# Kernel tuning notes

Hardware: AMD Instinct MI355X
Metric: run time of the kernel (lower is better)

## Reference

```python
import jax, jax.numpy as jnp
import numpy as np

NUM_GROUPS = 32
EPS = 1e-6


def group_norm(x, gamma, beta):
    # x: [b, c, n]
    b, c, n = x.shape
    xg = x.reshape(b, NUM_GROUPS, (c // NUM_GROUPS) * n)
    mean = xg.mean(axis=-1, keepdims=True)
    var = xg.var(axis=-1, keepdims=True)
    xg = (xg - mean) * jax.lax.rsqrt(var + EPS)
    x = xg.reshape(b, c, n)
    return x * gamma[None, :, None] + beta[None, :, None]


def conv1x1(x, w, bias):
    # x: [b, c, n], w: [out, in], bias: [out]
    return jnp.einsum('oc,bcn->bon', w, x) + bias[None, :, None]


def setup_inputs() -> dict:
    key = jax.random.key(0)
    ks = jax.random.split(key, 12)
    b, c, n = 16, 512, 2048
    scale = 1.0 / np.sqrt(c)
    inp = {
        'x': jax.random.normal(ks[0], (b, c, n), dtype=jnp.float32),
        'gn_gamma': jnp.ones((c,), dtype=jnp.float32),
        'gn_beta': jnp.zeros((c,), dtype=jnp.float32),
        'wq': jax.random.normal(ks[1], (c, c), dtype=jnp.float32) * scale,
        'bq': jnp.zeros((c,), dtype=jnp.float32),
        'wk': jax.random.normal(ks[2], (c, c), dtype=jnp.float32) * scale,
        'bk': jnp.zeros((c,), dtype=jnp.float32),
        'wv': jax.random.normal(ks[3], (c, c), dtype=jnp.float32) * scale,
        'bv': jnp.zeros((c,), dtype=jnp.float32),
        'wo': jax.random.normal(ks[4], (c, c), dtype=jnp.float32) * scale,
        'bo': jnp.zeros((c,), dtype=jnp.float32),
    }
    return inp


def reference(x, gn_gamma, gn_beta, wq, bq, wk, bk, wv, bv, wo, bo):
    # x: [b, c, n]
    c = x.shape[1]
    h = group_norm(x, gn_gamma, gn_beta)
    q = conv1x1(h, wq, bq)  # [b, c, n]
    k = conv1x1(h, wk, bk)  # [b, c, n]
    v = conv1x1(h, wv, bv)  # [b, c, n]
    # scores: q^T k  -> [b, n_q, n_kv]
    scores = jnp.einsum('bcn,bcm->bnm', q, k) * (c ** -0.5)
    attn = jax.nn.softmax(scores, axis=-1)  # softmax over keys (dim=2)
    # h = v @ attn^T  -> [b, c, n_q]
    out = jnp.einsum('bcm,bnm->bcn', v, attn)
    out = conv1x1(out, wo, bo)
    return x + out
```

## Files before the change

### kernel.cpp

```cpp
#include <hip/hip_runtime.h>
#include <hip/hip_bf16.h>
#include <math.h>

#define Bb 16
#define Cc 512
#define Nn 2048

typedef unsigned short u16;
typedef __attribute__((ext_vector_type(8))) short bf16x8;
typedef __attribute__((ext_vector_type(4))) float f32x4;

typedef __attribute__((address_space(3))) unsigned as3_u32;
typedef __attribute__((address_space(1))) const unsigned as1_u32;

__device__ __forceinline__ float b2f(u16 u){ unsigned x = ((unsigned)u) << 16; return __builtin_bit_cast(float, x); }
__device__ __forceinline__ u16 f2b(float f){
  unsigned x = __builtin_bit_cast(unsigned, f);
  x += 0x7fffu + ((x >> 16) & 1u);
  return (u16)(x >> 16);
}

__device__ __forceinline__ void gload16(const u16* g, u16* l){
  __builtin_amdgcn_global_load_lds((as1_u32*)(uintptr_t)(const void*)g,
                                   (as3_u32*)(uintptr_t)(void*)l, 16, 0, 0);
}

#define BAR() do{ __builtin_amdgcn_s_barrier(); asm volatile("" ::: "memory"); }while(0)
#define WAITV4() asm volatile("s_waitcnt vmcnt(4)" ::: "memory")
#define WAITV0() asm volatile("s_waitcnt vmcnt(0)" ::: "memory")

__global__ __launch_bounds__(256) void k_cvt(const float* __restrict__ s0, const float* __restrict__ s1,
                                             const float* __restrict__ s2,
                                             u16* __restrict__ d0, u16* __restrict__ d1, u16* __restrict__ d2){
  const float* s = (blockIdx.z == 0) ? s0 : (blockIdx.z == 1) ? s1 : s2;
  u16* d = (blockIdx.z == 0) ? d0 : (blockIdx.z == 1) ? d1 : d2;
  int i = blockIdx.x * 256 + threadIdx.x;
  float4 v = ((const float4*)s)[i];
  ushort4 o; o.x = f2b(v.x); o.y = f2b(v.y); o.z = f2b(v.z); o.w = f2b(v.w);
  ((ushort4*)d)[i] = o;
}

__global__ __launch_bounds__(256) void k_gn(const float* __restrict__ x,
                                            const float* __restrict__ gamma,
                                            const float* __restrict__ beta,
                                            u16* __restrict__ h){
  int bid = blockIdx.x;
  int b = bid >> 5, g = bid & 31;
  const float4* xv = (const float4*)(x + ((size_t)b * Cc + g * 16) * Nn);
  u16* hp = h + ((size_t)b * Cc + g * 16) * Nn;
  int t = threadIdx.x;
  float s = 0.f, ss = 0.f;
#pragma unroll 4
  for (int it = 0; it < 32; ++it){
    float4 v = xv[it * 256 + t];
    s  += v.x + v.y + v.z + v.w;
    ss += v.x * v.x + v.y * v.y + v.z * v.z + v.w * v.w;
  }
#pragma unroll
  for (int o = 32; o >= 1; o >>= 1){ s += __shfl_xor(s, o); ss += __shfl_xor(ss, o); }
  __shared__ float rs[4], rss[4];
  int w = t >> 6;
  if ((t & 63) == 0){ rs[w] = s; rss[w] = ss; }
  __syncthreads();
  s  = rs[0] + rs[1] + rs[2] + rs[3];
  ss = rss[0] + rss[1] + rss[2] + rss[3];
  float mean = s * (1.f / 32768.f);
  float var  = ss * (1.f / 32768.f) - mean * mean;
  float inv  = rsqrtf(var + 1e-6f);
#pragma unroll 4
  for (int it = 0; it < 32; ++it){
    int idx = it * 256 + t;
    float4 u = xv[idx];
    int ch = g * 16 + (idx >> 9);
    float ga = gamma[ch] * inv, be = beta[ch];
    ushort4 o;
    o.x = f2b((u.x - mean) * ga + be);
    o.y = f2b((u.y - mean) * ga + be);
    o.z = f2b((u.z - mean) * ga + be);
    o.w = f2b((u.w - mean) * ga + be);
    ((ushort4*)hp)[idx] = o;
  }
}

__global__ __launch_bounds__(256) void k_tr(const u16* __restrict__ h, u16* __restrict__ ht){
  __shared__ u16 lds[64 * 65];
  int b = blockIdx.z;
  int n0 = blockIdx.x * 64, c0 = blockIdx.y * 64;
  const u16* src = h + (size_t)b * Cc * Nn;
  u16* dst = ht + (size_t)b * Nn * Cc;
  int t = threadIdx.x;
  int jc = (t & 7) << 3;
  int r  = t >> 3;
#pragma unroll
  for (int it = 0; it < 2; ++it){
    int rr = r + it * 32;
    uint4 vv = *(const uint4*)(src + (size_t)(c0 + rr) * Nn + n0 + jc);
    u16* pv = (u16*)&vv;
#pragma unroll
    for (int e = 0; e < 8; ++e) lds[(jc + e) * 65 + rr] = pv[e];
  }
  __syncthreads();
#pragma unroll
  for (int it = 0; it < 2; ++it){
    int rn = r + it * 32;
    u16 tmp[8];
#pragma unroll
    for (int e = 0; e < 8; ++e) tmp[e] = lds[rn * 65 + jc + e];
    *(uint4*)(dst + (size_t)(n0 + rn) * Cc + c0 + jc) = *(const uint4*)tmp;
  }
}

#define GSLOT 16384

__device__ __forceinline__ void gemm256(const u16* __restrict__ A, int lda,
                                        const u16* __restrict__ B, int ldb, int K,
                                        u16* __restrict__ lds, f32x4 (&acc)[8][4]){
  const int tid = threadIdx.x;
  const int w = tid >> 6, lane = tid & 63;
  const int lr = lane & 15, lk = lane >> 4;
  const int wr = w >> 2, wc = w & 3;

  const int swzc = lk ^ ((lr >> 1) & 3);
  const int aoff = (wr * 128 + lr) * 32 + 8 * swzc;
  const int boff = 8192 + (wc * 64 + lr) * 32 + 8 * swzc;

  const int idx0 = w * 128 + lane;
  const int idx1 = idx0 + 64;
  const int r0s = idx0 >> 2, r1s = idx1 >> 2;
  const int c0 = (idx0 & 3) ^ ((r0s >> 1) & 3);
  const int c1 = (idx1 & 3) ^ ((r1s >> 1) & 3);
  const u16* gA0 = A + (size_t)r0s * lda + 8 * c0;
  const u16* gA1 = A + (size_t)r1s * lda + 8 * c1;
  const u16* gB0 = B + (size_t)r0s * ldb + 8 * c0;
  const u16* gB1 = B + (size_t)r1s * ldb + 8 * c1;
  const int dst0 = w * 1024;
  const int dst1 = dst0 + 512;

#pragma unroll
  for (int i = 0; i < 8; ++i)
#pragma unroll
    for (int j = 0; j < 4; ++j){ f32x4 z = {0.f,0.f,0.f,0.f}; acc[i][j] = z; }

  const int NT = K >> 5;

  gload16(gA0,      lds + dst0);            gload16(gA1,      lds + dst1);
  gload16(gB0,      lds + 8192 + dst0);     gload16(gB1,      lds + 8192 + dst1);
  gload16(gA0 + 32, lds + GSLOT + dst0);    gload16(gA1 + 32, lds + GSLOT + dst1);
  gload16(gB0 + 32, lds + GSLOT + 8192 + dst0);
  gload16(gB1 + 32, lds + GSLOT + 8192 + dst1);
  WAITV4();
  BAR();

  int s = 0;
#pragma unroll 1
  for (int T = 0; T < NT; ++T){
    const u16* Asl = lds + s * GSLOT;
    int st = s + 2; if (st >= 3) st -= 3;
    u16* stl = lds + st * GSLOT;
    const bool pf = (T + 2) < NT;
    const int kk = (T + 2) << 5;

    bf16x8 a0[4], b0[4];
#pragma unroll
    for (int i = 0; i < 4; ++i) a0[i] = *(const bf16x8*)(Asl + aoff + i * 512);
#pragma unroll
    for (int j = 0; j < 4; ++j) b0[j] = *(const bf16x8*)(Asl + boff + j * 512);
    if (pf){ gload16(gA0 + kk, stl + dst0); gload16(gA1 + kk, stl + dst1); }
    BAR();
    __builtin_amdgcn_s_setprio(1);
#pragma unroll
    for (int i = 0; i < 4; ++i)
#pragma unroll
      for (int j = 0; j < 4; ++j)
        acc[i][j] = __builtin_amdgcn_mfma_f32_16x16x32_bf16(b0[j], a0[i], acc[i][j], 0, 0, 0);
    __builtin_amdgcn_s_setprio(0);
    BAR();

    bf16x8 a1[4];
#pragma unroll
    for (int i = 0; i < 4; ++i) a1[i] = *(const bf16x8*)(Asl + aoff + (i + 4) * 512);
    if (pf){ gload16(gB0 + kk, stl + 8192 + dst0); gload16(gB1 + kk, stl + 8192 + dst1); }
    BAR();
    __builtin_amdgcn_s_setprio(1);
#pragma unroll
    for (int i = 0; i < 4; ++i)
#pragma unroll
      for (int j = 0; j < 4; ++j)
        acc[i + 4][j] = __builtin_amdgcn_mfma_f32_16x16x32_bf16(b0[j], a1[i], acc[i + 4][j], 0, 0, 0);
    __builtin_amdgcn_s_setprio(0);
    if (pf){ WAITV4(); } else { WAITV0(); }
    BAR();
    s = (s + 1 == 3) ? 0 : s + 1;
  }
}

#define EPI_COORDS \
  int lane = threadIdx.x & 63, w = threadIdx.x >> 6; \
  int wr = w >> 2, wc = w & 3; \
  int lr = lane & 15; \
  int lk = lane >> 4; \
  int g4 = lk << 2; \
  (void)lk;

__global__ __launch_bounds__(512, 2) void k_qkt(const u16* __restrict__ ht,
                                                const u16* __restrict__ wqb, const u16* __restrict__ wkb,
                                                const float* __restrict__ bq, const float* __restrict__ bk,
                                                u16* __restrict__ qt, u16* __restrict__ kt){
  __shared__ u16 lds[3 * GSLOT];
  int z = blockIdx.z, b = z >> 1, p = z & 1;
  int m0 = blockIdx.x * 256, n0 = blockIdx.y * 256;
  const u16* A = ht + (size_t)b * Nn * Cc + (size_t)m0 * Cc;
  const u16* B = (p ? wkb : wqb) + (size_t)n0 * Cc;
  const float* bias = p ? bk : bq;
  u16* out = (p ? kt : qt) + (size_t)b * Nn * Cc;
  f32x4 acc[8][4];
  gemm256(A, Cc, B, Cc, Cc, lds, acc);
  EPI_COORDS
#pragma unroll
  for (int i = 0; i < 8; ++i){
    int row = m0 + wr * 128 + i * 16 + lr;
#pragma unroll
    for (int j = 0; j < 4; ++j){
      int coln = n0 + wc * 64 + j * 16 + g4;
      float4 bi = *(const float4*)(bias + coln);
      ushort4 o;
      o.x = f2b(acc[i][j][0] + bi.x);
      o.y = f2b(acc[i][j][1] + bi.y);
      o.z = f2b(acc[i][j][2] + bi.z);
      o.w = f2b(acc[i][j][3] + bi.w);
      *(ushort4*)(out + (size_t)row * Cc + coln) = o;
    }
  }
}

__global__ __launch_bounds__(512, 2) void k_vproj(const u16* __restrict__ wvb, const u16* __restrict__ ht,
                                                  const float* __restrict__ bv, u16* __restrict__ v){
  __shared__ u16 lds[3 * GSLOT];
  int b = blockIdx.z;
  int m0 = blockIdx.x * 256, n0 = blockIdx.y * 256;
  const u16* A = wvb + (size_t)m0 * Cc;
  const u16* B = ht + (size_t)b * Nn * Cc + (size_t)n0 * Cc;
  u16* out = v + (size_t)b * Cc * Nn;
  f32x4 acc[8][4];
  gemm256(A, Cc, B, Cc, Cc, lds, acc);
  EPI_COORDS
#pragma unroll
  for (int i = 0; i < 8; ++i){
    int row = m0 + wr * 128 + i * 16 + lr;
    float bi = bv[row];
#pragma unroll
    for (int j = 0; j < 4; ++j){
      int coln = n0 + wc * 64 + j * 16 + g4;
      ushort4 o;
      o.x = f2b(acc[i][j][0] + bi);
      o.y = f2b(acc[i][j][1] + bi);
      o.z = f2b(acc[i][j][2] + bi);
      o.w = f2b(acc[i][j][3] + bi);
      *(ushort4*)(out + (size_t)row * Nn + coln) = o;
    }
  }
}

__global__ __launch_bounds__(512, 2) void k_scores(const u16* __restrict__ qt, const u16* __restrict__ kt,
                                                   u16* __restrict__ p, float* __restrict__ lsum){
  __shared__ u16 lds[3 * GSLOT];
  __shared__ float sums[256][4];
  int bid = blockIdx.x;
  int swz = (bid & 7) * 128 + (bid >> 3);
  int b = swz >> 6, rem = swz & 63;
  int m0 = (rem & 7) * 256, n0 = (rem >> 3) * 256;
  const u16* A = qt + (size_t)b * Nn * Cc + (size_t)m0 * Cc;
  const u16* B = kt + (size_t)b * Nn * Cc + (size_t)n0 * Cc;
  u16* pb = p + (size_t)b * Nn * Nn;
  f32x4 acc[8][4];
  gemm256(A, Cc, B, Cc, Cc, lds, acc);
  const float scale = 0.044194173824159216f;
  EPI_COORDS
  float psum[8];
#pragma unroll
  for (int i = 0; i < 8; ++i) psum[i] = 0.f;
#pragma unroll
  for (int i = 0; i < 8; ++i){
    int row = m0 + wr * 128 + i * 16 + lr;
#pragma unroll
    for (int j = 0; j < 4; ++j){
      int coln = n0 + wc * 64 + j * 16 + g4;
      float e0 = __expf(acc[i][j][0] * scale);
      float e1 = __expf(acc[i][j][1] * scale);
      float e2 = __expf(acc[i][j][2] * scale);
      float e3 = __expf(acc[i][j][3] * scale);
      psum[i] += (e0 + e1) + (e2 + e3);
      ushort4 o; o.x = f2b(e0); o.y = f2b(e1); o.z = f2b(e2); o.w = f2b(e3);
      *(ushort4*)(pb + (size_t)row * Nn + coln) = o;
    }
  }
#pragma unroll
  for (int i = 0; i < 8; ++i){
    psum[i] += __shfl_xor(psum[i], 16);
    psum[i] += __shfl_xor(psum[i], 32);
  }
  if (lk == 0){
#pragma unroll
    for (int i = 0; i < 8; ++i) sums[wr * 128 + i * 16 + lr][wc] = psum[i];
  }
  __syncthreads();
  int tid = threadIdx.x;
  if (tid < 256){
    float sv = sums[tid][0] + sums[tid][1] + sums[tid][2] + sums[tid][3];
    atomicAdd(lsum + (size_t)b * Nn + m0 + tid, sv);
  }
}

__global__ __launch_bounds__(512, 2) void k_pv(const u16* __restrict__ p, const u16* __restrict__ v,
                                               const float* __restrict__ lsum, u16* __restrict__ aot){
  __shared__ u16 lds[3 * GSLOT];
  int bid = blockIdx.x;
  int swz = (bid & 7) * 32 + (bid >> 3);
  int b = swz >> 4, rem = swz & 15;
  int m0 = (rem & 7) * 256, n0 = (rem >> 3) * 256;
  const u16* A = p + (size_t)b * Nn * Nn + (size_t)m0 * Nn;
  const u16* B = v + (size_t)b * Cc * Nn + (size_t)n0 * Nn;
  u16* out = aot + (size_t)b * Nn * Cc;
  f32x4 acc[8][4];
  gemm256(A, Nn, B, Nn, Nn, lds, acc);
  EPI_COORDS
#pragma unroll
  for (int i = 0; i < 8; ++i){
    int row = m0 + wr * 128 + i * 16 + lr;
    float linv = 1.0f / lsum[(size_t)b * Nn + row];
#pragma unroll
    for (int j = 0; j < 4; ++j){
      int coln = n0 + wc * 64 + j * 16 + g4;
      ushort4 o;
      o.x = f2b(acc[i][j][0] * linv);
      o.y = f2b(acc[i][j][1] * linv);
      o.z = f2b(acc[i][j][2] * linv);
      o.w = f2b(acc[i][j][3] * linv);
      *(ushort4*)(out + (size_t)row * Cc + coln) = o;
    }
  }
}

__global__ __launch_bounds__(512, 2) void k_proj(const u16* __restrict__ wob, const u16* __restrict__ aot,
                                                 const float* __restrict__ bo, const float* __restrict__ x,
                                                 float* __restrict__ out){
  __shared__ u16 lds[3 * GSLOT];
  int b = blockIdx.z;
  int m0 = blockIdx.x * 256, n0 = blockIdx.y * 256;
  const u16* A = wob + (size_t)m0 * Cc;
  const u16* B = aot + (size_t)b * Nn * Cc + (size_t)n0 * Cc;
  f32x4 acc[8][4];
  gemm256(A, Cc, B, Cc, Cc, lds, acc);
  size_t base = (size_t)b * Cc * Nn;
  EPI_COORDS
#pragma unroll
  for (int i = 0; i < 8; ++i){
    int row = m0 + wr * 128 + i * 16 + lr;
    float bi = bo[row];
#pragma unroll
    for (int j = 0; j < 4; ++j){
      int coln = n0 + wc * 64 + j * 16 + g4;
      size_t idx = base + (size_t)row * Nn + coln;
      float4 xv = *(const float4*)(x + idx);
      float4 o;
      o.x = xv.x + bi + acc[i][j][0];
      o.y = xv.y + bi + acc[i][j][1];
      o.z = xv.z + bi + acc[i][j][2];
      o.w = xv.w + bi + acc[i][j][3];
      *(float4*)(out + idx) = o;
    }
  }
}

extern "C" void kernel_launch(void* const* d_in, const int* in_sizes, int n_in,
                              void* d_out, int out_size, void* d_ws, size_t ws_size,
                              hipStream_t stream){
  const float* x     = (const float*)d_in[0];
  const float* gamma = (const float*)d_in[1];
  const float* beta  = (const float*)d_in[2];
  const float* wq = (const float*)d_in[3];
  const float* bq = (const float*)d_in[4];
  const float* wk = (const float*)d_in[5];
  const float* bk = (const float*)d_in[6];
  const float* wv = (const float*)d_in[7];
  const float* bv = (const float*)d_in[8];
  const float* wo = (const float*)d_in[9];
  const float* bo = (const float*)d_in[10];
  float* out = (float*)d_out;

  char* ws = (char*)d_ws;
  const size_t MB = 1048576ull;
  u16* P   = (u16*)ws;
  u16* h   = (u16*)ws;
  u16* ht  = (u16*)(ws + 32 * MB);
  u16* wqb = (u16*)(ws + 64 * MB);
  u16* wkb = wqb + 262144;
  u16* wvb = wqb + 524288;
  u16* qt  = (u16*)(ws + 128 * MB);
  u16* kt  = (u16*)(ws + 160 * MB);
  u16* v   = (u16*)(ws + 192 * MB);
  u16* wob = (u16*)(ws + 224 * MB);
  float* lsum = (float*)(ws + 225 * MB);
  u16* aot = qt;

  k_cvt<<<dim3(256, 1, 3), 256, 0, stream>>>(wq, wk, wv, wqb, wkb, wvb);
  k_cvt<<<dim3(256, 1, 1), 256, 0, stream>>>(wo, wo, wo, wob, wob, wob);
  k_gn<<<dim3(512), 256, 0, stream>>>(x, gamma, beta, h);
  k_tr<<<dim3(32, 8, 16), 256, 0, stream>>>(h, ht);
  k_qkt<<<dim3(8, 2, 32), 512, 0, stream>>>(ht, wqb, wkb, bq, bk, qt, kt);
  k_vproj<<<dim3(2, 8, 16), 512, 0, stream>>>(wvb, ht, bv, v);
  hipMemsetAsync(lsum, 0, (size_t)Bb * Nn * sizeof(float), stream);
  k_scores<<<dim3(1024), 512, 0, stream>>>(qt, kt, P, lsum);
  k_pv<<<dim3(256), 512, 0, stream>>>(P, v, lsum, aot);
  k_proj<<<dim3(2, 8, 16), 512, 0, stream>>>(wob, aot, bo, x, out);
}
```

Before: 337.4 us.

## Restructure shared GEMM to 64-wide K tiles with double-buffered quarter-stage prefetch

The common 256x256 bf16 GEMM core moves from a triple-buffered 32-wide K step to a double-buffered 64-wide K step. Each iteration is split into four MFMA quadrants, and loads for the next tiles are issued in halves between them, with a new XOR swizzle over 8 column chunks. The aim is fewer barriers and waits per unit of K and more MFMA work between synchronisations. The cost is tighter prefetch distance, since only two buffers are in flight, and LDS per block goes from 96KB to 128KB, which may affect two-blocks-per-CU occupancy.

```diff
diff --git a/kernel.cpp b/kernel.cpp
--- a/kernel.cpp
+++ b/kernel.cpp
@@ -110,7 +110,7 @@
   }
 }
 
-#define GSLOT 16384
+#define GSLOT 32768
 
 __device__ __forceinline__ void gemm256(const u16* __restrict__ A, int lda,
                                         const u16* __restrict__ B, int ldb, int K,
@@ -120,78 +120,120 @@
   const int lr = lane & 15, lk = lane >> 4;
   const int wr = w >> 2, wc = w & 3;
 
-  const int swzc = lk ^ ((lr >> 1) & 3);
-  const int aoff = (wr * 128 + lr) * 32 + 8 * swzc;
-  const int boff = 8192 + (wc * 64 + lr) * 32 + 8 * swzc;
-
-  const int idx0 = w * 128 + lane;
-  const int idx1 = idx0 + 64;
-  const int r0s = idx0 >> 2, r1s = idx1 >> 2;
-  const int c0 = (idx0 & 3) ^ ((r0s >> 1) & 3);
-  const int c1 = (idx1 & 3) ^ ((r1s >> 1) & 3);
-  const u16* gA0 = A + (size_t)r0s * lda + 8 * c0;
-  const u16* gA1 = A + (size_t)r1s * lda + 8 * c1;
-  const u16* gB0 = B + (size_t)r0s * ldb + 8 * c0;
-  const u16* gB1 = B + (size_t)r1s * ldb + 8 * c1;
-  const int dst0 = w * 1024;
-  const int dst1 = dst0 + 512;
+  const int sw0 = ((lk    ) ^ (lr & 7)) << 3;
+  const int sw1 = ((lk + 4) ^ (lr & 7)) << 3;
+  const int arow = (wr * 128 + lr) * 64;
+  const int brow = 16384 + (wc * 64 + lr) * 64;
+
+  const int r0 = tid >> 3, c0 = tid & 7;
+  const size_t offA0 = (size_t)r0 * lda + (size_t)((c0 ^ (r0 & 7)) << 3);
+  const size_t offA1 = offA0 + (size_t)64 * lda;
+  const size_t offB0 = (size_t)r0 * ldb + (size_t)((c0 ^ (r0 & 7)) << 3);
+  const size_t offB1 = offB0 + (size_t)64 * ldb;
+  const int d0 = tid * 8, d1 = tid * 8 + 4096;
+
+#define STGA(h, T, bu) do{ const u16* gp = A + (size_t)(T) * 64 + (size_t)(h) * 128 * lda; \
+    u16* lp = lds + (bu) * GSLOT + (h) * 8192; \
+    gload16(gp + offA0, lp + d0); gload16(gp + offA1, lp + d1); }while(0)
+#define STGB(h, T, bu) do{ const u16* gp = B + (size_t)(T) * 64 + (size_t)(h) * 128 * ldb; \
+    u16* lp = lds + (bu) * GSLOT + 16384 + (h) * 8192; \
+    gload16(gp + offB0, lp + d0); gload16(gp + offB1, lp + d1); }while(0)
 
 #pragma unroll
   for (int i = 0; i < 8; ++i)
 #pragma unroll
     for (int j = 0; j < 4; ++j){ f32x4 z = {0.f,0.f,0.f,0.f}; acc[i][j] = z; }
 
-  const int NT = K >> 5;
-
-  gload16(gA0,      lds + dst0);            gload16(gA1,      lds + dst1);
-  gload16(gB0,      lds + 8192 + dst0);     gload16(gB1,      lds + 8192 + dst1);
-  gload16(gA0 + 32, lds + GSLOT + dst0);    gload16(gA1 + 32, lds + GSLOT + dst1);
-  gload16(gB0 + 32, lds + GSLOT + 8192 + dst0);
-  gload16(gB1 + 32, lds + GSLOT + 8192 + dst1);
-  WAITV4();
+  const int NT = K >> 6;
+
+  STGA(0, 0, 0); STGA(1, 0, 0); STGB(0, 0, 0); STGB(1, 0, 0);
+  if (NT > 1){ STGB(0, 1, 1); STGA(0, 1, 1); WAITV4(); }
+  else { WAITV0(); }
   BAR();
 
-  int s = 0;
+  bf16x8 a[4][2], b[4][2];
+
 #pragma unroll 1
   for (int T = 0; T < NT; ++T){
-    const u16* Asl = lds + s * GSLOT;
-    int st = s + 2; if (st >= 3) st -= 3;
-    u16* stl = lds + st * GSLOT;
-    const bool pf = (T + 2) < NT;
-    const int kk = (T + 2) << 5;
-
-    bf16x8 a0[4], b0[4];
-#pragma unroll
-    for (int i = 0; i < 4; ++i) a0[i] = *(const bf16x8*)(Asl + aoff + i * 512);
-#pragma unroll
-    for (int j = 0; j < 4; ++j) b0[j] = *(const bf16x8*)(Asl + boff + j * 512);
-    if (pf){ gload16(gA0 + kk, stl + dst0); gload16(gA1 + kk, stl + dst1); }
+    const u16* cur = lds + (T & 1) * GSLOT;
+    const int nb = (T + 1) & 1, cb = T & 1;
+    const bool p1 = (T + 1) < NT, p2 = (T + 2) < NT;
+
+#pragma unroll
+    for (int i = 0; i < 4; ++i){
+      a[i][0] = *(const bf16x8*)(cur + arow + i * 1024 + sw0);
+      a[i][1] = *(const bf16x8*)(cur + arow + i * 1024 + sw1);
+    }
+#pragma unroll
+    for (int j = 0; j < 2; ++j){
+      b[j][0] = *(const bf16x8*)(cur + brow + j * 1024 + sw0);
+      b[j][1] = *(const bf16x8*)(cur + brow + j * 1024 + sw1);
+    }
+    if (p1) STGB(1, T + 1, nb);
     BAR();
     __builtin_amdgcn_s_setprio(1);
 #pragma unroll
     for (int i = 0; i < 4; ++i)
 #pragma unroll
-      for (int j = 0; j < 4; ++j)
-        acc[i][j] = __builtin_amdgcn_mfma_f32_16x16x32_bf16(b0[j], a0[i], acc[i][j], 0, 0, 0);
+      for (int j = 0; j < 2; ++j)
+#pragma unroll
+        for (int ks = 0; ks < 2; ++ks)
+          acc[i][j] = __builtin_amdgcn_mfma_f32_16x16x32_bf16(b[j][ks], a[i][ks], acc[i][j], 0, 0, 0);
     __builtin_amdgcn_s_setprio(0);
     BAR();
 
-    bf16x8 a1[4];
-#pragma unroll
-    for (int i = 0; i < 4; ++i) a1[i] = *(const bf16x8*)(Asl + aoff + (i + 4) * 512);
-    if (pf){ gload16(gB0 + kk, stl + 8192 + dst0); gload16(gB1 + kk, stl + 8192 + dst1); }
+#pragma unroll
+    for (int j = 2; j < 4; ++j){
+      b[j][0] = *(const bf16x8*)(cur + brow + j * 1024 + sw0);
+      b[j][1] = *(const bf16x8*)(cur + brow + j * 1024 + sw1);
+    }
+    if (p1) STGA(1, T + 1, nb);
     BAR();
     __builtin_amdgcn_s_setprio(1);
 #pragma unroll
     for (int i = 0; i < 4; ++i)
 #pragma unroll
-      for (int j = 0; j < 4; ++j)
-        acc[i + 4][j] = __builtin_amdgcn_mfma_f32_16x16x32_bf16(b0[j], a1[i], acc[i + 4][j], 0, 0, 0);
+      for (int j = 2; j < 4; ++j)
+#pragma unroll
+        for (int ks = 0; ks < 2; ++ks)
+          acc[i][j] = __builtin_amdgcn_mfma_f32_16x16x32_bf16(b[j][ks], a[i][ks], acc[i][j], 0, 0, 0);
     __builtin_amdgcn_s_setprio(0);
-    if (pf){ WAITV4(); } else { WAITV0(); }
-    BAR();
-    s = (s + 1 == 3) ? 0 : s + 1;
-  }
+    BAR();
+
+#pragma unroll
+    for (int i = 0; i < 4; ++i){
+      a[i][0] = *(const bf16x8*)(cur + arow + 4096 + i * 1024 + sw0);
+      a[i][1] = *(const bf16x8*)(cur + arow + 4096 + i * 1024 + sw1);
+    }
+    if (p2) STGB(0, T + 2, cb);
+    BAR();
+    __builtin_amdgcn_s_setprio(1);
+#pragma unroll
+    for (int i = 0; i < 4; ++i)
+#pragma unroll
+      for (int j = 0; j < 2; ++j)
+#pragma unroll
+        for (int ks = 0; ks < 2; ++ks)
+          acc[4 + i][j] = __builtin_amdgcn_mfma_f32_16x16x32_bf16(b[j][ks], a[i][ks], acc[4 + i][j], 0, 0, 0);
+    __builtin_amdgcn_s_setprio(0);
+    BAR();
+
+    if (p2) STGA(0, T + 2, cb);
+    BAR();
+    __builtin_amdgcn_s_setprio(1);
+#pragma unroll
+    for (int i = 0; i < 4; ++i)
+#pragma unroll
+      for (int j = 2; j < 4; ++j)
+#pragma unroll
+        for (int ks = 0; ks < 2; ++ks)
+          acc[4 + i][j] = __builtin_amdgcn_mfma_f32_16x16x32_bf16(b[j][ks], a[i][ks], acc[4 + i][j], 0, 0, 0);
+    __builtin_amdgcn_s_setprio(0);
+    if (p2){ WAITV4(); } else if (p1){ WAITV0(); }
+    BAR();
+  }
+#undef STGA
+#undef STGB
 }
 
 #define EPI_COORDS \
@@ -206,7 +248,7 @@
                                                 const u16* __restrict__ wqb, const u16* __restrict__ wkb,
                                                 const float* __restrict__ bq, const float* __restrict__ bk,
                                                 u16* __restrict__ qt, u16* __restrict__ kt){
-  __shared__ u16 lds[3 * GSLOT];
+  __shared__ u16 lds[2 * GSLOT];
   int z = blockIdx.z, b = z >> 1, p = z & 1;
   int m0 = blockIdx.x * 256, n0 = blockIdx.y * 256;
   const u16* A = ht + (size_t)b * Nn * Cc + (size_t)m0 * Cc;
@@ -235,7 +277,7 @@
 
 __global__ __launch_bounds__(512, 2) void k_vproj(const u16* __restrict__ wvb, const u16* __restrict__ ht,
                                                   const float* __restrict__ bv, u16* __restrict__ v){
-  __shared__ u16 lds[3 * GSLOT];
+  __shared__ u16 lds[2 * GSLOT];
   int b = blockIdx.z;
   int m0 = blockIdx.x * 256, n0 = blockIdx.y * 256;
   const u16* A = wvb + (size_t)m0 * Cc;
@@ -263,7 +305,7 @@
 
 __global__ __launch_bounds__(512, 2) void k_scores(const u16* __restrict__ qt, const u16* __restrict__ kt,
                                                    u16* __restrict__ p, float* __restrict__ lsum){
-  __shared__ u16 lds[3 * GSLOT];
+  __shared__ u16 lds[2 * GSLOT];
   __shared__ float sums[256][4];
   int bid = blockIdx.x;
   int swz = (bid & 7) * 128 + (bid >> 3);
@@ -313,7 +355,7 @@
 
 __global__ __launch_bounds__(512, 2) void k_pv(const u16* __restrict__ p, const u16* __restrict__ v,
                                                const float* __restrict__ lsum, u16* __restrict__ aot){
-  __shared__ u16 lds[3 * GSLOT];
+  __shared__ u16 lds[2 * GSLOT];
   int bid = blockIdx.x;
   int swz = (bid & 7) * 32 + (bid >> 3);
   int b = swz >> 4, rem = swz & 15;
@@ -344,7 +386,7 @@
 __global__ __launch_bounds__(512, 2) void k_proj(const u16* __restrict__ wob, const u16* __restrict__ aot,
                                                  const float* __restrict__ bo, const float* __restrict__ x,
                                                  float* __restrict__ out){
-  __shared__ u16 lds[3 * GSLOT];
+  __shared__ u16 lds[2 * GSLOT];
   int b = blockIdx.z;
   int m0 = blockIdx.x * 256, n0 = blockIdx.y * 256;
   const u16* A = wob + (size_t)m0 * Cc;
```

Result: faster. 330.1 us (-2.2%).
